# Optimization experiments

Measured on AMD Instinct MI355X. Metric: run time of the kernel, lower is better.

Reference implementation:

```python
import jax, jax.numpy as jnp
import numpy as np

C = 256
CQK = C // 8  # query/key projection dim (in_dim // 8)
B, H, W = 4, 64, 64


def setup_inputs() -> dict:
    key = jax.random.key(0)
    ks = jax.random.split(key, 7)
    scale = 0.05
    x = jax.random.normal(ks[0], (B, C, H, W), dtype=jnp.float32)
    Wq = jax.random.normal(ks[1], (CQK, C), dtype=jnp.float32) * scale
    bq = jax.random.normal(ks[2], (CQK,), dtype=jnp.float32) * scale
    Wk = jax.random.normal(ks[3], (CQK, C), dtype=jnp.float32) * scale
    bk = jax.random.normal(ks[4], (CQK,), dtype=jnp.float32) * scale
    Wv = jax.random.normal(ks[5], (C, C), dtype=jnp.float32) * scale
    bv = jax.random.normal(ks[6], (C,), dtype=jnp.float32) * scale
    return {"x": x, "Wq": Wq, "bq": bq, "Wk": Wk, "bk": bk, "Wv": Wv, "bv": bv}


def reference(x, Wq, bq, Wk, bk, Wv, bv):
    b, c, h, w = x.shape
    n = h * w
    xf = x.reshape(b, c, n)  # [B, C, N]
    # 1x1 convs == per-pixel linear maps over channels
    q = jnp.einsum('dc,bcn->bnd', Wq, xf) + bq[None, None, :]   # [B, N, C/8]
    k = jnp.einsum('dc,bcn->bdn', Wk, xf) + bk[None, :, None]   # [B, C/8, N]
    v = jnp.einsum('dc,bcn->bdn', Wv, xf) + bv[None, :, None]   # [B, C, N]
    energy = jnp.einsum('bnd,bdm->bnm', q, k)                    # [B, N, N]
    attention = jax.nn.softmax(energy, axis=-1)                  # softmax over keys
    # out = V @ attention^T  (torch: bmm(proj_value, attention.permute(0,2,1)))
    out = jnp.einsum('bdm,bnm->bdn', v, attention)               # [B, C, N]
    return out.reshape(b, c, h, w) + x
```

## Files before the change

kernel.cpp:

```cpp
#include <hip/hip_runtime.h>
#include <math.h>

#define BATCH 4
#define CH    256
#define NPIX  4096
#define DQK   32

typedef short          s16;
typedef unsigned int   uint_t;
typedef __attribute__((ext_vector_type(8))) short short8;
typedef __attribute__((ext_vector_type(4))) float floatx4;
typedef __attribute__((ext_vector_type(16))) float floatx16;

__device__ __forceinline__ s16 f2bf(float f) {
  union { float f; uint_t u; } v; v.f = f;
  return (s16)((v.u + 0x8000u) >> 16);
}
__device__ __forceinline__ uint_t pk2(float a, float b) {
  union { float f; uint_t u; } x, y; x.f = a; y.f = b;
  return (((y.u + 0x8000u) >> 16) << 16) | ((x.u + 0x8000u) >> 16);
}

__global__ __launch_bounds__(256) void prepack(
    const float* __restrict__ Wq, const float* __restrict__ bq,
    const float* __restrict__ Wk, const float* __restrict__ bk,
    const float* __restrict__ Wv, const float* __restrict__ bv,
    s16* __restrict__ Wbf, float* __restrict__ Bsw)
{
  const int gid = blockIdx.x * 256 + threadIdx.x;
  const int e0  = gid * 4;
  const int row = e0 >> 8, col = e0 & 255;
  const float* src = (row < 32) ? Wq + (size_t)row * 256
                   : (row < 64) ? Wk + (size_t)(row - 32) * 256
                                : Wv + (size_t)(row - 64) * 256;
  float4 f = *(const float4*)(src + col);
  uint2 o; o.x = pk2(f.x, f.y); o.y = pk2(f.z, f.w);
  *(uint2*)(Wbf + e0) = o;
  if (gid < 320)
    Bsw[gid] = (gid < 32) ? bq[gid] : (gid < 64) ? bk[gid - 32] : bv[gid - 64];
}

__global__ __launch_bounds__(256, 2) void proj_mfma(
    const float* __restrict__ x, const s16* __restrict__ Wbf,
    const float* __restrict__ Bsw,
    s16* __restrict__ Qw, s16* __restrict__ Kw, s16* __restrict__ Vw)
{
  const int b  = blockIdx.x >> 7;
  const int n0 = (blockIdx.x & 127) << 5;
  const int t  = threadIdx.x;

  __shared__ s16 Xs[32][264];
  __shared__ s16 Os[256][40];

  const float* xb = x + (size_t)b * CH * NPIX + n0;
  #pragma unroll
  for (int i = 0; i < 2; ++i) {
    int task = i * 256 + t;
    int ncg  = task & 7;
    int kcg  = task >> 3;
    const float* src = xb + (size_t)(kcg * 4) * NPIX + ncg * 4;
    float rows[4][4];
    *(float4*)&rows[0][0] = *(const float4*)(src);
    *(float4*)&rows[1][0] = *(const float4*)(src + NPIX);
    *(float4*)&rows[2][0] = *(const float4*)(src + 2 * NPIX);
    *(float4*)&rows[3][0] = *(const float4*)(src + 3 * NPIX);
    #pragma unroll
    for (int c = 0; c < 4; ++c) {
      uint2 pk;
      pk.x = pk2(rows[0][c], rows[1][c]);
      pk.y = pk2(rows[2][c], rows[3][c]);
      *(uint2*)&Xs[ncg * 4 + c][kcg * 4] = pk;
    }
  }
  __syncthreads();

  const int w    = t >> 6;
  const int l15  = t & 15;
  const int quad = (t & 63) >> 4;

  floatx4 acc[5][2];
  #pragma unroll
  for (int si = 0; si < 5; ++si)
    #pragma unroll
    for (int nt = 0; nt < 2; ++nt) acc[si][nt] = (floatx4){0.f, 0.f, 0.f, 0.f};

  short8 afc[5], afn[5];
  #pragma unroll
  for (int si = 0; si < 5; ++si) {
    const int s = w + si * 4;
    afc[si] = *(const short8*)(Wbf + (size_t)(s * 16 + l15) * 256 + quad * 8);
  }
  for (int kc = 0; kc < 8; ++kc) {
    const int k0  = kc * 32;
    const int kn0 = (kc < 7) ? k0 + 32 : 0;
    #pragma unroll
    for (int si = 0; si < 5; ++si) {
      const int s = w + si * 4;
      afn[si] = *(const short8*)(Wbf + (size_t)(s * 16 + l15) * 256 + kn0 + quad * 8);
    }
    short8 bf[2];
    #pragma unroll
    for (int nt = 0; nt < 2; ++nt)
      bf[nt] = *(const short8*)&Xs[l15 + 16 * nt][k0 + quad * 8];
    #pragma unroll
    for (int si = 0; si < 5; ++si)
      #pragma unroll
      for (int nt = 0; nt < 2; ++nt)
        acc[si][nt] = __builtin_amdgcn_mfma_f32_16x16x32_bf16(afc[si], bf[nt], acc[si][nt], 0, 0, 0);
    #pragma unroll
    for (int si = 0; si < 5; ++si) afc[si] = afn[si];
  }

  #pragma unroll
  for (int si = 0; si < 5; ++si) {
    const int s = w + si * 4;
    float4 bb = *(const float4*)(Bsw + 16 * s + quad * 4);
    #pragma unroll
    for (int nt = 0; nt < 2; ++nt) {
      const int px  = 16 * nt + l15;
      float v0 = acc[si][nt][0] + bb.x;
      float v1 = acc[si][nt][1] + bb.y;
      float v2 = acc[si][nt][2] + bb.z;
      float v3 = acc[si][nt][3] + bb.w;
      if (s < 4) {
        s16* dst = (s < 2) ? Qw : Kw;
        int d0 = (s & 1) * 16 + quad * 4;
        uint2 pq; pq.x = pk2(v0, v1); pq.y = pk2(v2, v3);
        *(uint2*)(dst + ((size_t)b * NPIX + n0 + px) * DQK + d0) = pq;
      } else {
        const int c0 = (s - 4) * 16 + quad * 4;
        Os[c0 + 0][px] = f2bf(v0);
        Os[c0 + 1][px] = f2bf(v1);
        Os[c0 + 2][px] = f2bf(v2);
        Os[c0 + 3][px] = f2bf(v3);
      }
    }
  }
  __syncthreads();
  #pragma unroll
  for (int rep = 0; rep < 4; ++rep) {
    const int task = rep * 256 + t;
    const int fid  = task >> 6;
    const int ln   = task & 63;
    const int c    = fid >> 1;
    const int sl   = fid & 1;
    const int row  = c * 32 + (ln & 31);
    const int col  = sl * 16 + (ln >> 5) * 8;
    *(uint4*)(Vw + (((size_t)b * 8 + c) * 256 + (n0 >> 4) + sl) * 512 + ln * 8) =
        *(const uint4*)&Os[row][col];
  }
}

__global__ __launch_bounds__(1024, 4) void attn_mfma(
    const s16* __restrict__ Qw, const s16* __restrict__ Kw,
    const s16* __restrict__ Vt, const float* __restrict__ x,
    float* __restrict__ out)
{
  const int bi = blockIdx.x;
  const int b  = bi & 3;
  const int qt = bi >> 2;
  const int n0 = qt * 64;
  const int t  = threadIdx.x;
  const int w    = t >> 6;
  const int lane = t & 63;
  const int l15  = t & 15;
  const int quad = lane >> 4;
  const int l31  = t & 31;
  const int lh   = lane >> 5;
  const int l7   = t & 7;
  const int sw   = w & 7;
  const int sq   = w >> 3;
  const int kh   = sq;

  __shared__ s16  Pt[2][64][128];
  __shared__ float Lsum[64][8];
  __shared__ float Ored[8][32][64];

  const s16* qbase = Qw + ((size_t)b * NPIX + n0 + sq * 32) * DQK;
  short8 qb[2];
  #pragma unroll
  for (int tq = 0; tq < 2; ++tq)
    qb[tq] = *(const short8*)(qbase + (size_t)(16 * tq + l15) * DQK + quad * 8);

  floatx16 o[2];
  #pragma unroll
  for (int i = 0; i < 16; ++i) { o[0][i] = 0.f; o[1][i] = 0.f; }
  float l_part[2] = {0.f, 0.f};

  const s16* kbase = Kw + (size_t)b * NPIX * DQK;
  const s16* vtb   = Vt + ((size_t)(b * 8 + sw) * 256) * 512 + lane * 8;

  short8 ka_c, ka_n, va[4];
  ka_c = *(const short8*)(kbase + (size_t)(16 * sw + l15) * DQK + quad * 8);
  #pragma unroll
  for (int ks = 0; ks < 4; ++ks)
    va[ks] = *(const short8*)(vtb + (size_t)(ks + 4 * kh) * 512);

  const int wslot = (((2 * sw + (quad >> 1)) ^ l7) << 3) + (quad & 1) * 4;

  {
    floatx4 sacc[2];
    #pragma unroll
    for (int tq = 0; tq < 2; ++tq)
      sacc[tq] = __builtin_amdgcn_mfma_f32_16x16x32_bf16(
                   ka_c, qb[tq], (floatx4){0.f, 0.f, 0.f, 0.f}, 0, 0, 0);
    ka_n = *(const short8*)(kbase + (size_t)(128 + 16 * sw + l15) * DQK + quad * 8);
    #pragma unroll
    for (int tq = 0; tq < 2; ++tq) {
      float p0 = __expf(fminf(sacc[tq][0], 60.f));
      float p1 = __expf(fminf(sacc[tq][1], 60.f));
      float p2 = __expf(fminf(sacc[tq][2], 60.f));
      float p3 = __expf(fminf(sacc[tq][3], 60.f));
      l_part[tq] += (p0 + p1) + (p2 + p3);
      uint2 pk; pk.x = pk2(p0, p1); pk.y = pk2(p2, p3);
      *(uint2*)&Pt[0][sq * 32 + 16 * tq + l15][wslot] = pk;
    }
    ka_c = ka_n;
  }
  __syncthreads();

  for (int kt = 0; kt < 32; ++kt) {
    const int buf = kt & 1;

    short8 pb[4][2];
    #pragma unroll
    for (int ks = 0; ks < 4; ++ks) {
      const int rslot = ((2 * (ks + 4 * kh) + lh) ^ l7) << 3;
      pb[ks][0] = *(const short8*)&Pt[buf][l31     ][rslot];
      pb[ks][1] = *(const short8*)&Pt[buf][32 + l31][rslot];
    }

    if (kt < 31) {
      floatx4 sacc[2];
      #pragma unroll
      for (int tq = 0; tq < 2; ++tq)
        sacc[tq] = __builtin_amdgcn_mfma_f32_16x16x32_bf16(
                     ka_c, qb[tq], (floatx4){0.f, 0.f, 0.f, 0.f}, 0, 0, 0);
      const int mn2 = (kt < 30) ? (kt + 2) * 128 : 0;
      ka_n = *(const short8*)(kbase + (size_t)(mn2 + 16 * sw + l15) * DQK + quad * 8);
      #pragma unroll
      for (int tq = 0; tq < 2; ++tq) {
        float p0 = __expf(fminf(sacc[tq][0], 60.f));
        float p1 = __expf(fminf(sacc[tq][1], 60.f));
        float p2 = __expf(fminf(sacc[tq][2], 60.f));
        float p3 = __expf(fminf(sacc[tq][3], 60.f));
        l_part[tq] += (p0 + p1) + (p2 + p3);
        uint2 pk; pk.x = pk2(p0, p1); pk.y = pk2(p2, p3);
        *(uint2*)&Pt[buf ^ 1][sq * 32 + 16 * tq + l15][wslot] = pk;
      }
      ka_c = ka_n;
    }

    __builtin_amdgcn_s_setprio(1);
    #pragma unroll
    for (int ks = 0; ks < 4; ++ks) {
      o[0] = __builtin_amdgcn_mfma_f32_32x32x16_bf16(va[ks], pb[ks][0], o[0], 0, 0, 0);
      o[1] = __builtin_amdgcn_mfma_f32_32x32x16_bf16(va[ks], pb[ks][1], o[1], 0, 0, 0);
    }
    __builtin_amdgcn_s_setprio(0);

    const int sn = ((kt + 1) & 31) * 8;
    #pragma unroll
    for (int ks = 0; ks < 4; ++ks)
      va[ks] = *(const short8*)(vtb + (size_t)(sn + ks + 4 * kh) * 512);

    __syncthreads();
  }

  #pragma unroll
  for (int tq = 0; tq < 2; ++tq) {
    l_part[tq] += __shfl_xor(l_part[tq], 16);
    l_part[tq] += __shfl_xor(l_part[tq], 32);
  }
  if (quad == 0) {
    #pragma unroll
    for (int tq = 0; tq < 2; ++tq) Lsum[sq * 32 + 16 * tq + l15][sw] = l_part[tq];
  }
  if (kh == 1) {
    #pragma unroll
    for (int r = 0; r < 16; ++r) {
      const int chrow = (r & 3) + 8 * (r >> 2) + 4 * lh;
      Ored[sw][chrow][l31]      = o[0][r];
      Ored[sw][chrow][32 + l31] = o[1][r];
    }
  }
  __syncthreads();

  if (kh == 0) {
    const int q0 = l31, q1 = 32 + l31;
    float4 a0 = *(const float4*)&Lsum[q0][0];
    float4 a1 = *(const float4*)&Lsum[q0][4];
    float4 b0 = *(const float4*)&Lsum[q1][0];
    float4 b1 = *(const float4*)&Lsum[q1][4];
    float inv0 = 1.f / (((a0.x + a0.y) + (a0.z + a0.w)) +
                        ((a1.x + a1.y) + (a1.z + a1.w)));
    float inv1 = 1.f / (((b0.x + b0.y) + (b0.z + b0.w)) +
                        ((b1.x + b1.y) + (b1.z + b1.w)));
    #pragma unroll
    for (int r = 0; r < 16; ++r) {
      const int chrow = (r & 3) + 8 * (r >> 2) + 4 * lh;
      const int ch = sw * 32 + chrow;
      const float s0 = o[0][r] + Ored[sw][chrow][l31];
      const float s1 = o[1][r] + Ored[sw][chrow][32 + l31];
      const size_t off0 = ((size_t)b * CH + ch) * NPIX + n0 + q0;
      const size_t off1 = ((size_t)b * CH + ch) * NPIX + n0 + q1;
      out[off0] = fmaf(s0, inv0, x[off0]);
      out[off1] = fmaf(s1, inv1, x[off1]);
    }
  }
}

extern "C" void kernel_launch(void* const* d_in, const int* in_sizes, int n_in,
                              void* d_out, int out_size, void* d_ws, size_t ws_size,
                              hipStream_t stream) {
  (void)in_sizes; (void)n_in; (void)out_size; (void)ws_size;
  const float* x  = (const float*)d_in[0];
  const float* Wq = (const float*)d_in[1];
  const float* bq = (const float*)d_in[2];
  const float* Wk = (const float*)d_in[3];
  const float* bk = (const float*)d_in[4];
  const float* Wv = (const float*)d_in[5];
  const float* bv = (const float*)d_in[6];
  float* out = (float*)d_out;

  unsigned char* ws = (unsigned char*)d_ws;
  s16*   Qw  = (s16*)ws;
  s16*   Kw  = (s16*)(ws + (size_t)1 * 1024 * 1024);
  s16*   Vt  = (s16*)(ws + (size_t)2 * 1024 * 1024);
  s16*   Wbf = (s16*)(ws + (size_t)10 * 1024 * 1024);
  float* Bsw = (float*)(ws + (size_t)10 * 1024 * 1024 + 256 * 1024);

  hipLaunchKernelGGL(prepack, dim3(80), dim3(256), 0, stream,
                     Wq, bq, Wk, bk, Wv, bv, Wbf, Bsw);
  hipLaunchKernelGGL(proj_mfma, dim3(512), dim3(256), 0, stream,
                     x, Wbf, Bsw, Qw, Kw, Vt);
  hipLaunchKernelGGL(attn_mfma, dim3(256), dim3(1024), 0, stream,
                     Qw, Kw, Vt, x, out);
}
```

Measured before the change: 136.0 us.

## Remap PV waves to 64-channel by 32-key tiles for P-fragment reuse

The PV stage is re-split across the 16 waves. Each wave now covers 64 channels (two 32-channel sub-blocks) over a quarter of each key tile, where before it covered 32 channels over half. Every P fragment loaded from LDS now feeds two MFMAs, which halves the per-wave LDS reads of P and doubles the accumulator registers. The price is a four-way split-K reduction done in shared memory in several stages with extra barriers, plus higher register pressure that may reduce occupancy.

New measurement: 138.8 us. 1.02x slower.

```diff
diff --git a/kernel.cpp b/kernel.cpp
--- a/kernel.cpp
+++ b/kernel.cpp
@@ -170,11 +170,12 @@
   const int l7   = t & 7;
   const int sw   = w & 7;
   const int sq   = w >> 3;
-  const int kh   = sq;
+  const int cb   = w & 3;
+  const int kh   = w >> 2;
 
   __shared__ s16  Pt[2][64][128];
   __shared__ float Lsum[64][8];
-  __shared__ float Ored[8][32][64];
+  __shared__ float Ored[4][64][64];
 
   const s16* qbase = Qw + ((size_t)b * NPIX + n0 + sq * 32) * DQK;
   short8 qb[2];
@@ -182,19 +183,24 @@
   for (int tq = 0; tq < 2; ++tq)
     qb[tq] = *(const short8*)(qbase + (size_t)(16 * tq + l15) * DQK + quad * 8);
 
-  floatx16 o[2];
-  #pragma unroll
-  for (int i = 0; i < 16; ++i) { o[0][i] = 0.f; o[1][i] = 0.f; }
+  floatx16 o[2][2];
+  #pragma unroll
+  for (int i = 0; i < 16; ++i) {
+    o[0][0][i] = 0.f; o[0][1][i] = 0.f; o[1][0][i] = 0.f; o[1][1][i] = 0.f;
+  }
   float l_part[2] = {0.f, 0.f};
 
   const s16* kbase = Kw + (size_t)b * NPIX * DQK;
-  const s16* vtb   = Vt + ((size_t)(b * 8 + sw) * 256) * 512 + lane * 8;
-
-  short8 ka_c, ka_n, va[4];
+  const s16* vtb   = Vt + ((size_t)(b * 8 + 2 * cb) * 256) * 512 + lane * 8;
+
+  short8 ka_c, ka_n, va[2][2];
   ka_c = *(const short8*)(kbase + (size_t)(16 * sw + l15) * DQK + quad * 8);
   #pragma unroll
-  for (int ks = 0; ks < 4; ++ks)
-    va[ks] = *(const short8*)(vtb + (size_t)(ks + 4 * kh) * 512);
+  for (int csub = 0; csub < 2; ++csub)
+    #pragma unroll
+    for (int ks = 0; ks < 2; ++ks)
+      va[csub][ks] = *(const short8*)(vtb + (size_t)csub * 131072 +
+                                      (size_t)(2 * kh + ks) * 512);
 
   const int wslot = (((2 * sw + (quad >> 1)) ^ l7) << 3) + (quad & 1) * 4;
 
@@ -221,14 +227,6 @@
 
   for (int kt = 0; kt < 32; ++kt) {
     const int buf = kt & 1;
-
-    short8 pb[4][2];
-    #pragma unroll
-    for (int ks = 0; ks < 4; ++ks) {
-      const int rslot = ((2 * (ks + 4 * kh) + lh) ^ l7) << 3;
-      pb[ks][0] = *(const short8*)&Pt[buf][l31     ][rslot];
-      pb[ks][1] = *(const short8*)&Pt[buf][32 + l31][rslot];
-    }
 
     if (kt < 31) {
       floatx4 sacc[2];
@@ -252,17 +250,31 @@
     }
 
     __builtin_amdgcn_s_setprio(1);
-    #pragma unroll
-    for (int ks = 0; ks < 4; ++ks) {
-      o[0] = __builtin_amdgcn_mfma_f32_32x32x16_bf16(va[ks], pb[ks][0], o[0], 0, 0, 0);
-      o[1] = __builtin_amdgcn_mfma_f32_32x32x16_bf16(va[ks], pb[ks][1], o[1], 0, 0, 0);
+    {
+      const int rs0 = ((2 * (2 * kh + 0) + lh) ^ l7) << 3;
+      short8 p0a = *(const short8*)&Pt[buf][l31     ][rs0];
+      short8 p0b = *(const short8*)&Pt[buf][32 + l31][rs0];
+      o[0][0] = __builtin_amdgcn_mfma_f32_32x32x16_bf16(va[0][0], p0a, o[0][0], 0, 0, 0);
+      o[1][0] = __builtin_amdgcn_mfma_f32_32x32x16_bf16(va[1][0], p0a, o[1][0], 0, 0, 0);
+      o[0][1] = __builtin_amdgcn_mfma_f32_32x32x16_bf16(va[0][0], p0b, o[0][1], 0, 0, 0);
+      o[1][1] = __builtin_amdgcn_mfma_f32_32x32x16_bf16(va[1][0], p0b, o[1][1], 0, 0, 0);
+      const int rs1 = ((2 * (2 * kh + 1) + lh) ^ l7) << 3;
+      short8 p1a = *(const short8*)&Pt[buf][l31     ][rs1];
+      short8 p1b = *(const short8*)&Pt[buf][32 + l31][rs1];
+      o[0][0] = __builtin_amdgcn_mfma_f32_32x32x16_bf16(va[0][1], p1a, o[0][0], 0, 0, 0);
+      o[1][0] = __builtin_amdgcn_mfma_f32_32x32x16_bf16(va[1][1], p1a, o[1][0], 0, 0, 0);
+      o[0][1] = __builtin_amdgcn_mfma_f32_32x32x16_bf16(va[0][1], p1b, o[0][1], 0, 0, 0);
+      o[1][1] = __builtin_amdgcn_mfma_f32_32x32x16_bf16(va[1][1], p1b, o[1][1], 0, 0, 0);
     }
     __builtin_amdgcn_s_setprio(0);
 
     const int sn = ((kt + 1) & 31) * 8;
     #pragma unroll
-    for (int ks = 0; ks < 4; ++ks)
-      va[ks] = *(const short8*)(vtb + (size_t)(sn + ks + 4 * kh) * 512);
+    for (int csub = 0; csub < 2; ++csub)
+      #pragma unroll
+      for (int ks = 0; ks < 2; ++ks)
+        va[csub][ks] = *(const short8*)(vtb + (size_t)csub * 131072 +
+                                        (size_t)(sn + 2 * kh + ks) * 512);
 
     __syncthreads();
   }
@@ -276,13 +288,54 @@
     #pragma unroll
     for (int tq = 0; tq < 2; ++tq) Lsum[sq * 32 + 16 * tq + l15][sw] = l_part[tq];
   }
+
   if (kh == 1) {
     #pragma unroll
-    for (int r = 0; r < 16; ++r) {
-      const int chrow = (r & 3) + 8 * (r >> 2) + 4 * lh;
-      Ored[sw][chrow][l31]      = o[0][r];
-      Ored[sw][chrow][32 + l31] = o[1][r];
-    }
+    for (int csub = 0; csub < 2; ++csub)
+      #pragma unroll
+      for (int qh = 0; qh < 2; ++qh)
+        #pragma unroll
+        for (int r = 0; r < 16; ++r) {
+          const int chrow = (r & 3) + 8 * (r >> 2) + 4 * lh;
+          Ored[cb][csub * 32 + chrow][qh * 32 + l31] = o[csub][qh][r];
+        }
+  }
+  __syncthreads();
+  if (kh == 0) {
+    #pragma unroll
+    for (int csub = 0; csub < 2; ++csub)
+      #pragma unroll
+      for (int qh = 0; qh < 2; ++qh)
+        #pragma unroll
+        for (int r = 0; r < 16; ++r) {
+          const int chrow = (r & 3) + 8 * (r >> 2) + 4 * lh;
+          o[csub][qh][r] += Ored[cb][csub * 32 + chrow][qh * 32 + l31];
+        }
+  }
+  __syncthreads();
+  if (kh == 3) {
+    #pragma unroll
+    for (int csub = 0; csub < 2; ++csub)
+      #pragma unroll
+      for (int qh = 0; qh < 2; ++qh)
+        #pragma unroll
+        for (int r = 0; r < 16; ++r) {
+          const int chrow = (r & 3) + 8 * (r >> 2) + 4 * lh;
+          Ored[cb][csub * 32 + chrow][qh * 32 + l31] = o[csub][qh][r];
+        }
+  }
+  __syncthreads();
+  if (kh == 2) {
+    #pragma unroll
+    for (int csub = 0; csub < 2; ++csub)
+      #pragma unroll
+      for (int qh = 0; qh < 2; ++qh)
+        #pragma unroll
+        for (int r = 0; r < 16; ++r) {
+          const int chrow = (r & 3) + 8 * (r >> 2) + 4 * lh;
+          o[csub][qh][r] += Ored[cb][csub * 32 + chrow][qh * 32 + l31];
+          Ored[cb][csub * 32 + chrow][qh * 32 + l31] = o[csub][qh][r];
+        }
   }
   __syncthreads();
 
@@ -297,16 +350,18 @@
     float inv1 = 1.f / (((b0.x + b0.y) + (b0.z + b0.w)) +
                         ((b1.x + b1.y) + (b1.z + b1.w)));
     #pragma unroll
-    for (int r = 0; r < 16; ++r) {
-      const int chrow = (r & 3) + 8 * (r >> 2) + 4 * lh;
-      const int ch = sw * 32 + chrow;
-      const float s0 = o[0][r] + Ored[sw][chrow][l31];
-      const float s1 = o[1][r] + Ored[sw][chrow][32 + l31];
-      const size_t off0 = ((size_t)b * CH + ch) * NPIX + n0 + q0;
-      const size_t off1 = ((size_t)b * CH + ch) * NPIX + n0 + q1;
-      out[off0] = fmaf(s0, inv0, x[off0]);
-      out[off1] = fmaf(s1, inv1, x[off1]);
-    }
+    for (int csub = 0; csub < 2; ++csub)
+      #pragma unroll
+      for (int r = 0; r < 16; ++r) {
+        const int chrow = (r & 3) + 8 * (r >> 2) + 4 * lh;
+        const int ch = (2 * cb + csub) * 32 + chrow;
+        const float s0 = o[csub][0][r] + Ored[cb][csub * 32 + chrow][q0];
+        const float s1 = o[csub][1][r] + Ored[cb][csub * 32 + chrow][q1];
+        const size_t off0 = ((size_t)b * CH + ch) * NPIX + n0 + q0;
+        const size_t off1 = ((size_t)b * CH + ch) * NPIX + n0 + q1;
+        out[off0] = fmaf(s0, inv0, x[off0]);
+        out[off1] = fmaf(s1, inv1, x[off1]);
+      }
   }
 }
 
```

## Fuse prepack, projection and attention into one cooperative kernel with grid syncs

Applied to the files above, without the earlier changes.

Merges the three kernels into a single cooperative launch of 256 blocks of 1024 threads. Each stage is separated by a grid-wide barrier and the stages share one shared-memory buffer. The projection stage now handles two 32-pixel tiles per block, one per 512-thread half. The Q weights and bias are pre-scaled by log2(e) so the softmax can use exp2f in place of __expf. This removes two kernel launch gaps, at the cost of grid-sync overhead and lower occupancy in the projection phase. It also depends on all 256 blocks fitting on the device at once.

Result: slower. 358.5 us (+163.5%).

```diff
diff --git a/kernel.cpp b/kernel.cpp
--- a/kernel.cpp
+++ b/kernel.cpp
@@ -1,5 +1,8 @@
 #include <hip/hip_runtime.h>
+#include <hip/hip_cooperative_groups.h>
 #include <math.h>
+
+namespace cg = cooperative_groups;
 
 #define BATCH 4
 #define CH    256
@@ -21,291 +24,287 @@
   return (((y.u + 0x8000u) >> 16) << 16) | ((x.u + 0x8000u) >> 16);
 }
 
-__global__ __launch_bounds__(256) void prepack(
+__global__ __launch_bounds__(1024, 4) void sn_fused(
+    const float* __restrict__ x,
     const float* __restrict__ Wq, const float* __restrict__ bq,
     const float* __restrict__ Wk, const float* __restrict__ bk,
     const float* __restrict__ Wv, const float* __restrict__ bv,
-    s16* __restrict__ Wbf, float* __restrict__ Bsw)
+    s16* __restrict__ Wbf, float* __restrict__ Bsw,
+    s16* __restrict__ Qw, s16* __restrict__ Kw, s16* __restrict__ Vt,
+    float* __restrict__ out)
 {
-  const int gid = blockIdx.x * 256 + threadIdx.x;
-  const int e0  = gid * 4;
-  const int row = e0 >> 8, col = e0 & 255;
-  const float* src = (row < 32) ? Wq + (size_t)row * 256
-                   : (row < 64) ? Wk + (size_t)(row - 32) * 256
-                                : Wv + (size_t)(row - 64) * 256;
-  float4 f = *(const float4*)(src + col);
-  uint2 o; o.x = pk2(f.x, f.y); o.y = pk2(f.z, f.w);
-  *(uint2*)(Wbf + e0) = o;
-  if (gid < 320)
-    Bsw[gid] = (gid < 32) ? bq[gid] : (gid < 64) ? bk[gid - 32] : bv[gid - 64];
-}
-
-__global__ __launch_bounds__(256, 2) void proj_mfma(
-    const float* __restrict__ x, const s16* __restrict__ Wbf,
-    const float* __restrict__ Bsw,
-    s16* __restrict__ Qw, s16* __restrict__ Kw, s16* __restrict__ Vw)
-{
-  const int b  = blockIdx.x >> 7;
-  const int n0 = (blockIdx.x & 127) << 5;
-  const int t  = threadIdx.x;
-
-  __shared__ s16 Xs[32][264];
-  __shared__ s16 Os[256][40];
-
-  const float* xb = x + (size_t)b * CH * NPIX + n0;
-  #pragma unroll
-  for (int i = 0; i < 2; ++i) {
-    int task = i * 256 + t;
-    int ncg  = task & 7;
-    int kcg  = task >> 3;
-    const float* src = xb + (size_t)(kcg * 4) * NPIX + ncg * 4;
-    float rows[4][4];
-    *(float4*)&rows[0][0] = *(const float4*)(src);
-    *(float4*)&rows[1][0] = *(const float4*)(src + NPIX);
-    *(float4*)&rows[2][0] = *(const float4*)(src + 2 * NPIX);
-    *(float4*)&rows[3][0] = *(const float4*)(src + 3 * NPIX);
-    #pragma unroll
-    for (int c = 0; c < 4; ++c) {
-      uint2 pk;
-      pk.x = pk2(rows[0][c], rows[1][c]);
-      pk.y = pk2(rows[2][c], rows[3][c]);
-      *(uint2*)&Xs[ncg * 4 + c][kcg * 4] = pk;
-    }
+  cg::grid_group grid = cg::this_grid();
+  __shared__ __align__(16) unsigned char smem[100352];
+
+  const int bi   = blockIdx.x;
+  const int t    = threadIdx.x;
+  const int w    = t >> 6;
+  const int lane = t & 63;
+  const int l15  = t & 15;
+  const int quad = lane >> 4;
+
+  if (bi < 20) {
+    const float LOG2E = 1.4426950408889634f;
+    const int gid = bi * 1024 + t;
+    const int e0  = gid * 4;
+    const int row = e0 >> 8, col = e0 & 255;
+    const float* src = (row < 32) ? Wq + (size_t)row * 256
+                     : (row < 64) ? Wk + (size_t)(row - 32) * 256
+                                  : Wv + (size_t)(row - 64) * 256;
+    float4 f = *(const float4*)(src + col);
+    const float sc = (row < 32) ? LOG2E : 1.f;
+    uint2 o2; o2.x = pk2(f.x * sc, f.y * sc); o2.y = pk2(f.z * sc, f.w * sc);
+    *(uint2*)(Wbf + e0) = o2;
+    if (gid < 320)
+      Bsw[gid] = (gid < 32) ? bq[gid] * LOG2E
+               : (gid < 64) ? bk[gid - 32] : bv[gid - 64];
   }
-  __syncthreads();
-
-  const int w    = t >> 6;
-  const int l15  = t & 15;
-  const int quad = (t & 63) >> 4;
-
-  floatx4 acc[5][2];
-  #pragma unroll
-  for (int si = 0; si < 5; ++si)
-    #pragma unroll
-    for (int nt = 0; nt < 2; ++nt) acc[si][nt] = (floatx4){0.f, 0.f, 0.f, 0.f};
-
-  short8 afc[5], afn[5];
-  #pragma unroll
-  for (int si = 0; si < 5; ++si) {
-    const int s = w + si * 4;
-    afc[si] = *(const short8*)(Wbf + (size_t)(s * 16 + l15) * 256 + quad * 8);
-  }
-  for (int kc = 0; kc < 8; ++kc) {
-    const int k0  = kc * 32;
-    const int kn0 = (kc < 7) ? k0 + 32 : 0;
+  __threadfence();
+  grid.sync();
+
+  {
+    s16 (*Xs)[32][264] = reinterpret_cast<s16 (*)[32][264]>(smem);
+    s16 (*Os)[256][40] = reinterpret_cast<s16 (*)[256][40]>(smem + 33792);
+    const int g    = t >> 9;
+    const int tt   = t & 511;
+    const int w8   = w & 7;
+    const int wr   = w8 & 3;
+    const int nt   = w8 >> 2;
+    const int tile = 2 * bi + g;
+    const int pb   = tile >> 7;
+    const int n0p  = (tile & 127) << 5;
+
+    {
+      const int ncg = tt & 7;
+      const int kcg = tt >> 3;
+      const float* src = x + (size_t)pb * CH * NPIX + n0p +
+                         (size_t)(kcg * 4) * NPIX + ncg * 4;
+      float rows[4][4];
+      *(float4*)&rows[0][0] = *(const float4*)(src);
+      *(float4*)&rows[1][0] = *(const float4*)(src + NPIX);
+      *(float4*)&rows[2][0] = *(const float4*)(src + 2 * NPIX);
+      *(float4*)&rows[3][0] = *(const float4*)(src + 3 * NPIX);
+      #pragma unroll
+      for (int c = 0; c < 4; ++c) {
+        uint2 pk;
+        pk.x = pk2(rows[0][c], rows[1][c]);
+        pk.y = pk2(rows[2][c], rows[3][c]);
+        *(uint2*)&Xs[g][ncg * 4 + c][kcg * 4] = pk;
+      }
+    }
+    __syncthreads();
+
+    floatx4 acc[5];
+    #pragma unroll
+    for (int si = 0; si < 5; ++si) acc[si] = (floatx4){0.f, 0.f, 0.f, 0.f};
+
+    short8 afc[5], afn[5];
     #pragma unroll
     for (int si = 0; si < 5; ++si) {
-      const int s = w + si * 4;
-      afn[si] = *(const short8*)(Wbf + (size_t)(s * 16 + l15) * 256 + kn0 + quad * 8);
-    }
-    short8 bf[2];
-    #pragma unroll
-    for (int nt = 0; nt < 2; ++nt)
-      bf[nt] = *(const short8*)&Xs[l15 + 16 * nt][k0 + quad * 8];
-    #pragma unroll
-    for (int si = 0; si < 5; ++si)
-      #pragma unroll
-      for (int nt = 0; nt < 2; ++nt)
-        acc[si][nt] = __builtin_amdgcn_mfma_f32_16x16x32_bf16(afc[si], bf[nt], acc[si][nt], 0, 0, 0);
-    #pragma unroll
-    for (int si = 0; si < 5; ++si) afc[si] = afn[si];
-  }
-
-  #pragma unroll
-  for (int si = 0; si < 5; ++si) {
-    const int s = w + si * 4;
-    float4 bb = *(const float4*)(Bsw + 16 * s + quad * 4);
-    #pragma unroll
-    for (int nt = 0; nt < 2; ++nt) {
-      const int px  = 16 * nt + l15;
-      float v0 = acc[si][nt][0] + bb.x;
-      float v1 = acc[si][nt][1] + bb.y;
-      float v2 = acc[si][nt][2] + bb.z;
-      float v3 = acc[si][nt][3] + bb.w;
+      const int s = wr + si * 4;
+      afc[si] = *(const short8*)(Wbf + (size_t)(s * 16 + l15) * 256 + quad * 8);
+    }
+    for (int kc = 0; kc < 8; ++kc) {
+      const int k0  = kc * 32;
+      const int kn0 = (kc < 7) ? k0 + 32 : 0;
+      #pragma unroll
+      for (int si = 0; si < 5; ++si) {
+        const int s = wr + si * 4;
+        afn[si] = *(const short8*)(Wbf + (size_t)(s * 16 + l15) * 256 + kn0 + quad * 8);
+      }
+      short8 bf = *(const short8*)&Xs[g][l15 + 16 * nt][k0 + quad * 8];
+      #pragma unroll
+      for (int si = 0; si < 5; ++si)
+        acc[si] = __builtin_amdgcn_mfma_f32_16x16x32_bf16(afc[si], bf, acc[si], 0, 0, 0);
+      #pragma unroll
+      for (int si = 0; si < 5; ++si) afc[si] = afn[si];
+    }
+
+    #pragma unroll
+    for (int si = 0; si < 5; ++si) {
+      const int s = wr + si * 4;
+      float4 bb = *(const float4*)(Bsw + 16 * s + quad * 4);
+      const int px = 16 * nt + l15;
+      float v0 = acc[si][0] + bb.x;
+      float v1 = acc[si][1] + bb.y;
+      float v2 = acc[si][2] + bb.z;
+      float v3 = acc[si][3] + bb.w;
       if (s < 4) {
         s16* dst = (s < 2) ? Qw : Kw;
         int d0 = (s & 1) * 16 + quad * 4;
         uint2 pq; pq.x = pk2(v0, v1); pq.y = pk2(v2, v3);
-        *(uint2*)(dst + ((size_t)b * NPIX + n0 + px) * DQK + d0) = pq;
+        *(uint2*)(dst + ((size_t)pb * NPIX + n0p + px) * DQK + d0) = pq;
       } else {
         const int c0 = (s - 4) * 16 + quad * 4;
-        Os[c0 + 0][px] = f2bf(v0);
-        Os[c0 + 1][px] = f2bf(v1);
-        Os[c0 + 2][px] = f2bf(v2);
-        Os[c0 + 3][px] = f2bf(v3);
-      }
+        Os[g][c0 + 0][px] = f2bf(v0);
+        Os[g][c0 + 1][px] = f2bf(v1);
+        Os[g][c0 + 2][px] = f2bf(v2);
+        Os[g][c0 + 3][px] = f2bf(v3);
+      }
+    }
+    __syncthreads();
+    #pragma unroll
+    for (int rep = 0; rep < 2; ++rep) {
+      const int task = rep * 512 + tt;
+      const int fid  = task >> 6;
+      const int ln   = task & 63;
+      const int c    = fid >> 1;
+      const int sl   = fid & 1;
+      const int row  = c * 32 + (ln & 31);
+      const int col  = sl * 16 + (ln >> 5) * 8;
+      *(uint4*)(Vt + (((size_t)pb * 8 + c) * 256 + (n0p >> 4) + sl) * 512 + ln * 8) =
+          *(const uint4*)&Os[g][row][col];
     }
   }
-  __syncthreads();
-  #pragma unroll
-  for (int rep = 0; rep < 4; ++rep) {
-    const int task = rep * 256 + t;
-    const int fid  = task >> 6;
-    const int ln   = task & 63;
-    const int c    = fid >> 1;
-    const int sl   = fid & 1;
-    const int row  = c * 32 + (ln & 31);
-    const int col  = sl * 16 + (ln >> 5) * 8;
-    *(uint4*)(Vw + (((size_t)b * 8 + c) * 256 + (n0 >> 4) + sl) * 512 + ln * 8) =
-        *(const uint4*)&Os[row][col];
-  }
-}
-
-__global__ __launch_bounds__(1024, 4) void attn_mfma(
-    const s16* __restrict__ Qw, const s16* __restrict__ Kw,
-    const s16* __restrict__ Vt, const float* __restrict__ x,
-    float* __restrict__ out)
-{
-  const int bi = blockIdx.x;
-  const int b  = bi & 3;
-  const int qt = bi >> 2;
-  const int n0 = qt * 64;
-  const int t  = threadIdx.x;
-  const int w    = t >> 6;
-  const int lane = t & 63;
-  const int l15  = t & 15;
-  const int quad = lane >> 4;
-  const int l31  = t & 31;
-  const int lh   = lane >> 5;
-  const int l7   = t & 7;
-  const int sw   = w & 7;
-  const int sq   = w >> 3;
-  const int kh   = sq;
-
-  __shared__ s16  Pt[2][64][128];
-  __shared__ float Lsum[64][8];
-  __shared__ float Ored[8][32][64];
-
-  const s16* qbase = Qw + ((size_t)b * NPIX + n0 + sq * 32) * DQK;
-  short8 qb[2];
-  #pragma unroll
-  for (int tq = 0; tq < 2; ++tq)
-    qb[tq] = *(const short8*)(qbase + (size_t)(16 * tq + l15) * DQK + quad * 8);
-
-  floatx16 o[2];
-  #pragma unroll
-  for (int i = 0; i < 16; ++i) { o[0][i] = 0.f; o[1][i] = 0.f; }
-  float l_part[2] = {0.f, 0.f};
-
-  const s16* kbase = Kw + (size_t)b * NPIX * DQK;
-  const s16* vtb   = Vt + ((size_t)(b * 8 + sw) * 256) * 512 + lane * 8;
-
-  short8 ka_c, ka_n, va[4];
-  ka_c = *(const short8*)(kbase + (size_t)(16 * sw + l15) * DQK + quad * 8);
-  #pragma unroll
-  for (int ks = 0; ks < 4; ++ks)
-    va[ks] = *(const short8*)(vtb + (size_t)(ks + 4 * kh) * 512);
-
-  const int wslot = (((2 * sw + (quad >> 1)) ^ l7) << 3) + (quad & 1) * 4;
+  __threadfence();
+  grid.sync();
 
   {
-    floatx4 sacc[2];
+    s16   (*Pt)[64][128] = reinterpret_cast<s16 (*)[64][128]>(smem);
+    float (*Lsum)[8]     = reinterpret_cast<float (*)[8]>(smem + 32768);
+    float (*Ored)[32][64]= reinterpret_cast<float (*)[32][64]>(smem + 34816);
+
+    const int b  = bi & 3;
+    const int qt = bi >> 2;
+    const int n0 = qt * 64;
+    const int l31 = t & 31;
+    const int lh  = lane >> 5;
+    const int l7  = t & 7;
+    const int sw  = w & 7;
+    const int sq  = w >> 3;
+    const int kh  = sq;
+
+    const s16* qbase = Qw + ((size_t)b * NPIX + n0 + sq * 32) * DQK;
+    short8 qb[2];
     #pragma unroll
     for (int tq = 0; tq < 2; ++tq)
-      sacc[tq] = __builtin_amdgcn_mfma_f32_16x16x32_bf16(
-                   ka_c, qb[tq], (floatx4){0.f, 0.f, 0.f, 0.f}, 0, 0, 0);
-    ka_n = *(const short8*)(kbase + (size_t)(128 + 16 * sw + l15) * DQK + quad * 8);
-    #pragma unroll
-    for (int tq = 0; tq < 2; ++tq) {
-      float p0 = __expf(fminf(sacc[tq][0], 60.f));
-      float p1 = __expf(fminf(sacc[tq][1], 60.f));
-      float p2 = __expf(fminf(sacc[tq][2], 60.f));
-      float p3 = __expf(fminf(sacc[tq][3], 60.f));
-      l_part[tq] += (p0 + p1) + (p2 + p3);
-      uint2 pk; pk.x = pk2(p0, p1); pk.y = pk2(p2, p3);
-      *(uint2*)&Pt[0][sq * 32 + 16 * tq + l15][wslot] = pk;
-    }
-    ka_c = ka_n;
-  }
-  __syncthreads();
-
-  for (int kt = 0; kt < 32; ++kt) {
-    const int buf = kt & 1;
-
-    short8 pb[4][2];
-    #pragma unroll
-    for (int ks = 0; ks < 4; ++ks) {
-      const int rslot = ((2 * (ks + 4 * kh) + lh) ^ l7) << 3;
-      pb[ks][0] = *(const short8*)&Pt[buf][l31     ][rslot];
-      pb[ks][1] = *(const short8*)&Pt[buf][32 + l31][rslot];
-    }
-
-    if (kt < 31) {
+      qb[tq] = *(const short8*)(qbase + (size_t)(16 * tq + l15) * DQK + quad * 8);
+
+    floatx16 o[2];
+    #pragma unroll
+    for (int i = 0; i < 16; ++i) { o[0][i] = 0.f; o[1][i] = 0.f; }
+    float l_part[2] = {0.f, 0.f};
+
+    const s16* kbase = Kw + (size_t)b * NPIX * DQK;
+    const s16* vtb   = Vt + ((size_t)(b * 8 + sw) * 256) * 512 + lane * 8;
+
+    short8 ka_c, ka_n, va[4];
+    ka_c = *(const short8*)(kbase + (size_t)(16 * sw + l15) * DQK + quad * 8);
+    #pragma unroll
+    for (int ks = 0; ks < 4; ++ks)
+      va[ks] = *(const short8*)(vtb + (size_t)(ks + 4 * kh) * 512);
+
+    const int wslot = (((2 * sw + (quad >> 1)) ^ l7) << 3) + (quad & 1) * 4;
+
+    {
       floatx4 sacc[2];
       #pragma unroll
       for (int tq = 0; tq < 2; ++tq)
         sacc[tq] = __builtin_amdgcn_mfma_f32_16x16x32_bf16(
                      ka_c, qb[tq], (floatx4){0.f, 0.f, 0.f, 0.f}, 0, 0, 0);
-      const int mn2 = (kt < 30) ? (kt + 2) * 128 : 0;
-      ka_n = *(const short8*)(kbase + (size_t)(mn2 + 16 * sw + l15) * DQK + quad * 8);
+      ka_n = *(const short8*)(kbase + (size_t)(128 + 16 * sw + l15) * DQK + quad * 8);
       #pragma unroll
       for (int tq = 0; tq < 2; ++tq) {
-        float p0 = __expf(fminf(sacc[tq][0], 60.f));
-        float p1 = __expf(fminf(sacc[tq][1], 60.f));
-        float p2 = __expf(fminf(sacc[tq][2], 60.f));
-        float p3 = __expf(fminf(sacc[tq][3], 60.f));
+        float p0 = exp2f(fminf(sacc[tq][0], 86.f));
+        float p1 = exp2f(fminf(sacc[tq][1], 86.f));
+        float p2 = exp2f(fminf(sacc[tq][2], 86.f));
+        float p3 = exp2f(fminf(sacc[tq][3], 86.f));
         l_part[tq] += (p0 + p1) + (p2 + p3);
         uint2 pk; pk.x = pk2(p0, p1); pk.y = pk2(p2, p3);
-        *(uint2*)&Pt[buf ^ 1][sq * 32 + 16 * tq + l15][wslot] = pk;
+        *(uint2*)&Pt[0][sq * 32 + 16 * tq + l15][wslot] = pk;
       }
       ka_c = ka_n;
     }
-
-    __builtin_amdgcn_s_setprio(1);
-    #pragma unroll
-    for (int ks = 0; ks < 4; ++ks) {
-      o[0] = __builtin_amdgcn_mfma_f32_32x32x16_bf16(va[ks], pb[ks][0], o[0], 0, 0, 0);
-      o[1] = __builtin_amdgcn_mfma_f32_32x32x16_bf16(va[ks], pb[ks][1], o[1], 0, 0, 0);
-    }
-    __builtin_amdgcn_s_setprio(0);
-
-    const int sn = ((kt + 1) & 31) * 8;
-    #pragma unroll
-    for (int ks = 0; ks < 4; ++ks)
-      va[ks] = *(const short8*)(vtb + (size_t)(sn + ks + 4 * kh) * 512);
-
     __syncthreads();
-  }
-
-  #pragma unroll
-  for (int tq = 0; tq < 2; ++tq) {
-    l_part[tq] += __shfl_xor(l_part[tq], 16);
-    l_part[tq] += __shfl_xor(l_part[tq], 32);
-  }
-  if (quad == 0) {
-    #pragma unroll
-    for (int tq = 0; tq < 2; ++tq) Lsum[sq * 32 + 16 * tq + l15][sw] = l_part[tq];
-  }
-  if (kh == 1) {
-    #pragma unroll
-    for (int r = 0; r < 16; ++r) {
-      const int chrow = (r & 3) + 8 * (r >> 2) + 4 * lh;
-      Ored[sw][chrow][l31]      = o[0][r];
-      Ored[sw][chrow][32 + l31] = o[1][r];
-    }
-  }
-  __syncthreads();
-
-  if (kh == 0) {
-    const int q0 = l31, q1 = 32 + l31;
-    float4 a0 = *(const float4*)&Lsum[q0][0];
-    float4 a1 = *(const float4*)&Lsum[q0][4];
-    float4 b0 = *(const float4*)&Lsum[q1][0];
-    float4 b1 = *(const float4*)&Lsum[q1][4];
-    float inv0 = 1.f / (((a0.x + a0.y) + (a0.z + a0.w)) +
-                        ((a1.x + a1.y) + (a1.z + a1.w)));
-    float inv1 = 1.f / (((b0.x + b0.y) + (b0.z + b0.w)) +
-                        ((b1.x + b1.y) + (b1.z + b1.w)));
-    #pragma unroll
-    for (int r = 0; r < 16; ++r) {
-      const int chrow = (r & 3) + 8 * (r >> 2) + 4 * lh;
-      const int ch = sw * 32 + chrow;
-      const float s0 = o[0][r] + Ored[sw][chrow][l31];
-      const float s1 = o[1][r] + Ored[sw][chrow][32 + l31];
-      const size_t off0 = ((size_t)b * CH + ch) * NPIX + n0 + q0;
-      const size_t off1 = ((size_t)b * CH + ch) * NPIX + n0 + q1;
-      out[off0] = fmaf(s0, inv0, x[off0]);
-      out[off1] = fmaf(s1, inv1, x[off1]);
+
+    for (int kt = 0; kt < 32; ++kt) {
+      const int buf = kt & 1;
+
+      short8 pb[4][2];
+      #pragma unroll
+      for (int ks = 0; ks < 4; ++ks) {
+        const int rslot = ((2 * (ks + 4 * kh) + lh) ^ l7) << 3;
+        pb[ks][0] = *(const short8*)&Pt[buf][l31     ][rslot];
+        pb[ks][1] = *(const short8*)&Pt[buf][32 + l31][rslot];
+      }
+
+      if (kt < 31) {
+        floatx4 sacc[2];
+        #pragma unroll
+        for (int tq = 0; tq < 2; ++tq)
+          sacc[tq] = __builtin_amdgcn_mfma_f32_16x16x32_bf16(
+                       ka_c, qb[tq], (floatx4){0.f, 0.f, 0.f, 0.f}, 0, 0, 0);
+        const int mn2 = (kt < 30) ? (kt + 2) * 128 : 0;
+        ka_n = *(const short8*)(kbase + (size_t)(mn2 + 16 * sw + l15) * DQK + quad * 8);
+        #pragma unroll
+        for (int tq = 0; tq < 2; ++tq) {
+          float p0 = exp2f(fminf(sacc[tq][0], 86.f));
+          float p1 = exp2f(fminf(sacc[tq][1], 86.f));
+          float p2 = exp2f(fminf(sacc[tq][2], 86.f));
+          float p3 = exp2f(fminf(sacc[tq][3], 86.f));
+          l_part[tq] += (p0 + p1) + (p2 + p3);
+          uint2 pk; pk.x = pk2(p0, p1); pk.y = pk2(p2, p3);
+          *(uint2*)&Pt[buf ^ 1][sq * 32 + 16 * tq + l15][wslot] = pk;
+        }
+        ka_c = ka_n;
+      }
+
+      __builtin_amdgcn_s_setprio(1);
+      #pragma unroll
+      for (int ks = 0; ks < 4; ++ks) {
+        o[0] = __builtin_amdgcn_mfma_f32_32x32x16_bf16(va[ks], pb[ks][0], o[0], 0, 0, 0);
+        o[1] = __builtin_amdgcn_mfma_f32_32x32x16_bf16(va[ks], pb[ks][1], o[1], 0, 0, 0);
+      }
+      __builtin_amdgcn_s_setprio(0);
+
+      const int sn = ((kt + 1) & 31) * 8;
+      #pragma unroll
+      for (int ks = 0; ks < 4; ++ks)
+        va[ks] = *(const short8*)(vtb + (size_t)(sn + ks + 4 * kh) * 512);
+
+      __syncthreads();
+    }
+
+    #pragma unroll
+    for (int tq = 0; tq < 2; ++tq) {
+      l_part[tq] += __shfl_xor(l_part[tq], 16);
+      l_part[tq] += __shfl_xor(l_part[tq], 32);
+    }
+    if (quad == 0) {
+      #pragma unroll
+      for (int tq = 0; tq < 2; ++tq) Lsum[sq * 32 + 16 * tq + l15][sw] = l_part[tq];
+    }
+    if (kh == 1) {
+      #pragma unroll
+      for (int r = 0; r < 16; ++r) {
+        const int chrow = (r & 3) + 8 * (r >> 2) + 4 * lh;
+        Ored[sw][chrow][l31]      = o[0][r];
+        Ored[sw][chrow][32 + l31] = o[1][r];
+      }
+    }
+    __syncthreads();
+
+    if (kh == 0) {
+      const int q0 = l31, q1 = 32 + l31;
+      float4 a0 = *(const float4*)&Lsum[q0][0];
+      float4 a1 = *(const float4*)&Lsum[q0][4];
+      float4 b0 = *(const float4*)&Lsum[q1][0];
+      float4 b1 = *(const float4*)&Lsum[q1][4];
+      float inv0 = 1.f / (((a0.x + a0.y) + (a0.z + a0.w)) +
+                          ((a1.x + a1.y) + (a1.z + a1.w)));
+      float inv1 = 1.f / (((b0.x + b0.y) + (b0.z + b0.w)) +
+                          ((b1.x + b1.y) + (b1.z + b1.w)));
+      #pragma unroll
+      for (int r = 0; r < 16; ++r) {
+        const int chrow = (r & 3) + 8 * (r >> 2) + 4 * lh;
+        const int ch = sw * 32 + chrow;
+        const float s0 = o[0][r] + Ored[sw][chrow][l31];
+        const float s1 = o[1][r] + Ored[sw][chrow][32 + l31];
+        const size_t off0 = ((size_t)b * CH + ch) * NPIX + n0 + q0;
+        const size_t off1 = ((size_t)b * CH + ch) * NPIX + n0 + q1;
+        out[off0] = fmaf(s0, inv0, x[off0]);
+        out[off1] = fmaf(s1, inv1, x[off1]);
+      }
     }
   }
 }
@@ -330,10 +329,11 @@
   s16*   Wbf = (s16*)(ws + (size_t)10 * 1024 * 1024);
   float* Bsw = (float*)(ws + (size_t)10 * 1024 * 1024 + 256 * 1024);
 
-  hipLaunchKernelGGL(prepack, dim3(80), dim3(256), 0, stream,
-                     Wq, bq, Wk, bk, Wv, bv, Wbf, Bsw);
-  hipLaunchKernelGGL(proj_mfma, dim3(512), dim3(256), 0, stream,
-                     x, Wbf, Bsw, Qw, Kw, Vt);
-  hipLaunchKernelGGL(attn_mfma, dim3(256), dim3(1024), 0, stream,
-                     Qw, Kw, Vt, x, out);
+  void* args[] = {
+    (void*)&x, (void*)&Wq, (void*)&bq, (void*)&Wk, (void*)&bk,
+    (void*)&Wv, (void*)&bv, (void*)&Wbf, (void*)&Bsw,
+    (void*)&Qw, (void*)&Kw, (void*)&Vt, (void*)&out
+  };
+  hipLaunchCooperativeKernel(reinterpret_cast<const void*>(sn_fused),
+                             dim3(256), dim3(1024), args, 0, stream);
 }
```
